# Kernel optimization log

Hardware: AMD Instinct MI355X
Metric: run time of the kernel (lower is better)

The kernel has to match this reference:

```python
import jax, jax.numpy as jnp
import numpy as np

D_MODEL = 768
D_STATE = 16
D_CONV = 4
EXPAND = 2
N_LAYERS = 8
VOCAB = 512
MAXSEQ = 2048
BATCH = 8
SEQ = 2048
D_INNER = EXPAND * D_MODEL
N_EMO, N_STY, N_KEY, N_MODE = 8, 8, 12, 2


def setup_inputs() -> dict:
    key = jax.random.key(0)
    ks = jax.random.split(key, 32)
    def nrm(k, shape, s=0.02):
        return (jax.random.normal(k, shape) * s).astype(jnp.float32)
    inp = {}
    inp['tokens'] = jax.random.randint(ks[0], (BATCH, SEQ), 0, VOCAB)
    inp['emotion'] = jax.random.randint(ks[1], (BATCH,), 0, N_EMO)
    inp['style'] = jax.random.randint(ks[2], (BATCH,), 0, N_STY)
    inp['key_sig'] = jax.random.randint(ks[3], (BATCH,), 0, N_KEY)
    inp['mode'] = jax.random.randint(ks[4], (BATCH,), 0, N_MODE)
    inp['bpm'] = (jax.random.uniform(ks[5], (BATCH,)) * 140.0 + 60.0).astype(jnp.float32)
    inp['tok_emb'] = nrm(ks[6], (VOCAB, D_MODEL))
    inp['emo_emb'] = nrm(ks[7], (N_EMO, D_MODEL))
    inp['sty_emb'] = nrm(ks[8], (N_STY, D_MODEL))
    inp['key_emb'] = nrm(ks[9], (N_KEY, D_MODEL))
    inp['mode_emb'] = nrm(ks[10], (N_MODE, D_MODEL))
    inp['bpm_w'] = nrm(ks[11], (D_MODEL, 1))
    inp['bpm_b'] = jnp.zeros((D_MODEL,), jnp.float32)
    inp['cond_w'] = nrm(ks[12], (D_MODEL, 5 * D_MODEL))
    inp['cond_b'] = jnp.zeros((D_MODEL,), jnp.float32)
    inp['pos_emb'] = nrm(ks[13], (MAXSEQ, D_MODEL))
    inp['ln_g'] = jnp.ones((N_LAYERS, D_MODEL), jnp.float32)
    inp['ln_b'] = jnp.zeros((N_LAYERS, D_MODEL), jnp.float32)
    inp['in_w'] = nrm(ks[14], (N_LAYERS, 2 * D_INNER, D_MODEL))
    inp['conv_w'] = nrm(ks[15], (N_LAYERS, D_INNER, 1, D_CONV), 0.1)
    inp['xproj_w'] = nrm(ks[16], (N_LAYERS, 2 * D_STATE, D_INNER))
    inp['dt_w'] = nrm(ks[17], (N_LAYERS, D_INNER, D_STATE))
    inp['dt_b'] = jnp.zeros((N_LAYERS, D_INNER), jnp.float32)
    inp['bproj_w'] = nrm(ks[18], (N_LAYERS, D_INNER, D_STATE))
    inp['d_param'] = jnp.ones((N_LAYERS, D_INNER), jnp.float32)
    inp['out_w'] = nrm(ks[19], (N_LAYERS, D_MODEL, D_INNER))
    inp['final_g'] = jnp.ones((D_MODEL,), jnp.float32)
    inp['final_b'] = jnp.zeros((D_MODEL,), jnp.float32)
    inp['head_w'] = nrm(ks[20], (VOCAB, D_MODEL))
    inp['head_b'] = jnp.zeros((VOCAB,), jnp.float32)
    return inp


def _layernorm(x, g, b):
    mu = x.mean(-1, keepdims=True)
    v = ((x - mu) ** 2).mean(-1, keepdims=True)
    return (x - mu) * jax.lax.rsqrt(v + 1e-5) * g + b


def _silu(x):
    return x * jax.nn.sigmoid(x)


def _mamba_block(x, in_w, conv_w, xproj_w, dt_w, dt_b, bproj_w, d_param, out_w):
    B, L, _ = x.shape
    xz = x @ in_w.T                       # [B,L,2*di]
    xc, z = jnp.split(xz, 2, axis=-1)
    # causal depthwise conv1d: torch pads d_conv-1 both sides then slices [:L]
    xt = jnp.transpose(xc, (0, 2, 1))     # [B,di,L]
    xt = jax.lax.conv_general_dilated(xt, conv_w, (1,), [(D_CONV - 1, 0)],
                                      feature_group_count=D_INNER)
    xc = _silu(jnp.transpose(xt, (0, 2, 1)))   # [B,L,di]
    dt_raw, b_raw = jnp.split(xc @ xproj_w.T, 2, axis=-1)  # each [B,L,ds]
    delta = jnp.clip(jax.nn.softplus(dt_raw @ dt_w.T + dt_b), 1e-4, 1.0)  # [B,L,di]
    bp = b_raw @ bproj_w.T                 # [B,L,di]

    def step(h, inputs):
        d, u, bb = inputs
        h = h * (1.0 - d) + u * bb
        return h, h

    xs = (jnp.transpose(delta, (1, 0, 2)),
          jnp.transpose(xc, (1, 0, 2)),
          jnp.transpose(bp, (1, 0, 2)))    # time-major [L,B,di]
    h0 = jnp.zeros((B, D_INNER), x.dtype)
    _, ys = jax.lax.scan(step, h0, xs)
    y = jnp.transpose(ys, (1, 0, 2)) + d_param * xc
    y = y * _silu(z)
    return y @ out_w.T


def reference(tokens, emotion, style, key_sig, mode, bpm, tok_emb, emo_emb, sty_emb,
              key_emb, mode_emb, bpm_w, bpm_b, cond_w, cond_b, pos_emb, ln_g, ln_b,
              in_w, conv_w, xproj_w, dt_w, dt_b, bproj_w, d_param, out_w,
              final_g, final_b, head_w, head_b):
    B, L = tokens.shape
    cond = jnp.concatenate([
        emo_emb[emotion], sty_emb[style], key_emb[key_sig], mode_emb[mode],
        bpm[:, None] @ bpm_w.T + bpm_b], axis=-1)       # [B,5d]
    cond = cond @ cond_w.T + cond_b                      # [B,d]
    x = tok_emb[tokens] + cond[:, None, :] + pos_emb[:L][None]
    for i in range(N_LAYERS):
        res = x
        h = _layernorm(x, ln_g[i], ln_b[i])
        x = res + _mamba_block(h, in_w[i], conv_w[i], xproj_w[i], dt_w[i],
                               dt_b[i], bproj_w[i], d_param[i], out_w[i])
    x = _layernorm(x, final_g, final_b)
    return x @ head_w.T + head_b
```

## Files before the change

kernel.cpp:

```cpp
#include <hip/hip_runtime.h>
#include <cstdint>

#define BATCH 8
#define SEQ   2048
#define DM    768
#define DI    1536
#define DS    16
#define NL    8
#define NVOCAB 512
#define BT    (BATCH*SEQ)
#define NCHUNK 32
#define TC    (SEQ/NCHUNK)

typedef __attribute__((ext_vector_type(8))) short bf16x8;
typedef __attribute__((ext_vector_type(4))) float f32x4;

__device__ __forceinline__ unsigned short f2bf(float f){
  unsigned int u = __float_as_uint(f);
  u += 0x7fffu + ((u >> 16) & 1u);
  return (unsigned short)(u >> 16);
}
__device__ __forceinline__ float bf2f(unsigned short s){
  return __uint_as_float(((unsigned int)s) << 16);
}
__device__ __forceinline__ float sigm(float x){ return 1.0f/(1.0f + __expf(-x)); }
__device__ __forceinline__ float siluf(float x){ return x * sigm(x); }
__device__ __forceinline__ float fast_softplus(float x){
  return (x > 15.0f) ? x : __logf(1.0f + __expf(x));
}
__device__ __forceinline__ void async16(void* l, const void* g){
  __builtin_amdgcn_global_load_lds(
      (const __attribute__((address_space(1))) unsigned int*)g,
      (__attribute__((address_space(3))) unsigned int*)l, 16, 0, 0);
}
__device__ __forceinline__ float dot4(f32x4 a, f32x4 b){
  return fmaf(a[0],b[0], fmaf(a[1],b[1], fmaf(a[2],b[2], a[3]*b[3])));
}

__global__ void cvt_bf16_kernel(const float4* __restrict__ in, ushort4* __restrict__ out, int n4){
  int i = blockIdx.x*256 + threadIdx.x;
  int stride = gridDim.x*256;
  for(; i<n4; i+=stride){
    float4 v = in[i];
    ushort4 o; o.x=f2bf(v.x); o.y=f2bf(v.y); o.z=f2bf(v.z); o.w=f2bf(v.w);
    out[i]=o;
  }
}

__global__ __launch_bounds__(256) void cond_kernel(const int* __restrict__ emotion,
    const int* __restrict__ style, const int* __restrict__ keysig, const int* __restrict__ modei,
    const float* __restrict__ bpm, const float* __restrict__ emo_emb, const float* __restrict__ sty_emb,
    const float* __restrict__ key_emb, const float* __restrict__ mode_emb,
    const float* __restrict__ bpm_w, const float* __restrict__ bpm_b,
    const float* __restrict__ cond_w, const float* __restrict__ cond_b,
    float* __restrict__ cond_out){
  int b = blockIdx.y;
  int tid = threadIdx.x;
  __shared__ float vec[5*DM];
  int e = emotion[b], st = style[b], ks = keysig[b], md = modei[b];
  float bp = bpm[b];
  for(int j=tid; j<960; j+=256){
    int seg = j/192, o4 = j - seg*192;
    float4 v;
    if(seg==0)      v = reinterpret_cast<const float4*>(emo_emb + (long)e*DM)[o4];
    else if(seg==1) v = reinterpret_cast<const float4*>(sty_emb + (long)st*DM)[o4];
    else if(seg==2) v = reinterpret_cast<const float4*>(key_emb + (long)ks*DM)[o4];
    else if(seg==3) v = reinterpret_cast<const float4*>(mode_emb + (long)md*DM)[o4];
    else {
      float4 w = reinterpret_cast<const float4*>(bpm_w)[o4];
      float4 bb = reinterpret_cast<const float4*>(bpm_b)[o4];
      v = make_float4(fmaf(bp,w.x,bb.x), fmaf(bp,w.y,bb.y), fmaf(bp,w.z,bb.z), fmaf(bp,w.w,bb.w));
    }
    reinterpret_cast<float4*>(vec)[j] = v;
  }
  __syncthreads();
  int wid = tid>>6, lane = tid&63;
  int dm = blockIdx.x*4 + wid;
  const float4* w4 = reinterpret_cast<const float4*>(cond_w + (long)dm*(5*DM));
  const float4* v4 = reinterpret_cast<const float4*>(vec);
  float acc = 0.f;
  #pragma unroll 5
  for(int j=lane; j<960; j+=64){
    float4 w = w4[j], v = v4[j];
    acc = fmaf(w.x,v.x, fmaf(w.y,v.y, fmaf(w.z,v.z, fmaf(w.w,v.w, acc))));
  }
  #pragma unroll
  for(int off=32; off>0; off>>=1) acc += __shfl_xor(acc, off);
  if(lane==0) cond_out[b*DM + dm] = acc + cond_b[dm];
}

__global__ void embed_kernel(const int* __restrict__ tokens, const float* __restrict__ tok_emb,
    const float* __restrict__ cond, const float* __restrict__ pos_emb, float* __restrict__ x){
  int bt = blockIdx.x;
  int b = bt >> 11, t = bt & 2047;
  int tok = tokens[bt];
  const float4* te = reinterpret_cast<const float4*>(tok_emb + (long)tok*DM);
  const float4* ce = reinterpret_cast<const float4*>(cond + (long)b*DM);
  const float4* pe = reinterpret_cast<const float4*>(pos_emb + (long)t*DM);
  float4* xo = reinterpret_cast<float4*>(x + (long)bt*DM);
  int i = threadIdx.x;
  float4 a = te[i], c = ce[i], p = pe[i];
  xo[i] = make_float4(a.x+c.x+p.x, a.y+c.y+p.y, a.z+c.z+p.z, a.w+c.w+p.w);
}

__global__ __launch_bounds__(256) void ln_bf16_kernel(const float* __restrict__ x,
                     const float* __restrict__ g, const float* __restrict__ bta,
                     unsigned short* __restrict__ out){
  int row  = blockIdx.x*4 + (threadIdx.x >> 6);
  int lane = threadIdx.x & 63;
  const float* xr = x + (long)row*DM;
  float4 v[3];
  float sum=0.f, sq=0.f;
  #pragma unroll
  for(int i=0;i<3;i++){
    v[i] = *reinterpret_cast<const float4*>(xr + i*256 + lane*4);
    sum += v[i].x + v[i].y + v[i].z + v[i].w;
    sq  += v[i].x*v[i].x + v[i].y*v[i].y + v[i].z*v[i].z + v[i].w*v[i].w;
  }
  #pragma unroll
  for(int off=32; off>0; off>>=1){
    sum += __shfl_xor(sum, off);
    sq  += __shfl_xor(sq , off);
  }
  float mu  = sum * (1.0f/DM);
  float var = sq  * (1.0f/DM) - mu*mu;
  float rs  = rsqrtf(var + 1e-5f);
  unsigned short* orow = out + (long)row*DM;
  #pragma unroll
  for(int i=0;i<3;i++){
    int d = i*256 + lane*4;
    float4 gg = *reinterpret_cast<const float4*>(g + d);
    float4 bb = *reinterpret_cast<const float4*>(bta + d);
    ushort4 o;
    o.x = f2bf((v[i].x - mu)*rs*gg.x + bb.x);
    o.y = f2bf((v[i].y - mu)*rs*gg.y + bb.y);
    o.z = f2bf((v[i].z - mu)*rs*gg.z + bb.z);
    o.w = f2bf((v[i].w - mu)*rs*gg.w + bb.w);
    *reinterpret_cast<ushort4*>(orow + d) = o;
  }
}

template<int MODE>
__global__ __launch_bounds__(256) void gemm_lds(const unsigned short* __restrict__ A,
                                               const unsigned short* __restrict__ B,
                                               void* __restrict__ Cv,
                                               const float* __restrict__ bias,
                                               int K, int ldc){
  __shared__ short As[128*64];
  __shared__ short Bs[128*64];
  const short* Ap = (const short*)A;
  const short* Bp = (const short*)B;
  int tid  = threadIdx.x;
  int lane = tid & 63;
  int wid  = tid >> 6;

  int nbx = gridDim.x;
  int id  = blockIdx.y*nbx + blockIdx.x;
  int q   = (nbx*gridDim.y) >> 3;
  int swz = (id & 7)*q + (id >> 3);
  int bx  = swz % nbx, by = swz / nbx;
  int row0 = by*128;
  int col0 = bx*128;

  int srow[4], goff[4];
  #pragma unroll
  for(int j=0;j<4;j++){
    int c = j*256 + tid;
    int row = c>>3, s = c&7;
    srow[j] = row;
    goff[j] = (s ^ (row&7))*8;
  }

  int wr = (wid>>1)*64;
  int wc = (wid&1)*64;
  int fr = lane & 15;
  int kq = lane >> 4;
  int fx = fr & 7;

  f32x4 acc[4][4];
  #pragma unroll
  for(int m=0;m<4;m++)
    #pragma unroll
    for(int n=0;n<4;n++)
      acc[m][n] = (f32x4){0.f,0.f,0.f,0.f};

  for(int kt=0; kt<K; kt+=64){
    #pragma unroll
    for(int j=0;j<4;j++){
      int c = j*256 + tid;
      async16((char*)As + c*16, Ap + (long)(row0+srow[j])*K + kt + goff[j]);
      async16((char*)Bs + c*16, Bp + (long)(col0+srow[j])*K + kt + goff[j]);
    }
    __syncthreads();
    #pragma unroll
    for(int ks=0; ks<2; ks++){
      int sA = ((ks*4 + kq) ^ fx) * 8;
      bf16x8 av[4], bv[4];
      #pragma unroll
      for(int m=0;m<4;m++)
        av[m] = *reinterpret_cast<const bf16x8*>(As + (wr + m*16 + fr)*64 + sA);
      #pragma unroll
      for(int n=0;n<4;n++)
        bv[n] = *reinterpret_cast<const bf16x8*>(Bs + (wc + n*16 + fr)*64 + sA);
      #pragma unroll
      for(int m=0;m<4;m++)
        #pragma unroll
        for(int n=0;n<4;n++)
          acc[m][n] = __builtin_amdgcn_mfma_f32_16x16x32_bf16(av[m], bv[n], acc[m][n], 0, 0, 0);
    }
    __syncthreads();
  }

  int rr = (lane >> 4) << 2;
  int cc = lane & 15;
  #pragma unroll
  for(int m=0;m<4;m++){
    #pragma unroll
    for(int n=0;n<4;n++){
      int col = col0 + wc + n*16 + cc;
      #pragma unroll
      for(int i=0;i<4;i++){
        long idx = (long)(row0 + wr + m*16 + rr + i)*ldc + col;
        float v = acc[m][n][i];
        if(MODE==3)      ((unsigned short*)Cv)[idx] = f2bf(v);
        else if(MODE==1) ((float*)Cv)[idx] += v;
        else if(MODE==2) ((float*)Cv)[idx] = v + bias[col];
        else             ((float*)Cv)[idx] = v;
      }
    }
  }
}

__global__ __launch_bounds__(256) void xproj_kernel(const unsigned short* __restrict__ xz,
      const float* __restrict__ cw, const unsigned short* __restrict__ wbf,
      float* __restrict__ dtb){
  __shared__ unsigned short xcs[16][DI+8];
  __shared__ float pdt[4][16][32];
  int blk = blockIdx.x;
  int b  = blk >> 7;
  int t0 = (blk & 127) << 4;
  int tid = threadIdx.x;
  long base = ((long)b*SEQ + t0)*(2*DI);
  if(tid < 192){
    int d0 = tid*8;
    float cc0[8], cc1[8], cc2[8], cc3[8];
    #pragma unroll
    for(int j=0;j<8;j++){
      cc0[j]=cw[(d0+j)*4+0]; cc1[j]=cw[(d0+j)*4+1];
      cc2[j]=cw[(d0+j)*4+2]; cc3[j]=cw[(d0+j)*4+3];
    }
    float wm3[8], wm2[8], wm1[8];
    #pragma unroll
    for(int j=0;j<8;j++){ wm3[j]=0.f; wm2[j]=0.f; wm1[j]=0.f; }
    if(t0>0){
      bf16x8 v3 = *reinterpret_cast<const bf16x8*>(xz + base - 3*(2*DI) + d0);
      bf16x8 v2 = *reinterpret_cast<const bf16x8*>(xz + base - 2*(2*DI) + d0);
      bf16x8 v1 = *reinterpret_cast<const bf16x8*>(xz + base - 1*(2*DI) + d0);
      #pragma unroll
      for(int j=0;j<8;j++){
        wm3[j]=bf2f((unsigned short)v3[j]);
        wm2[j]=bf2f((unsigned short)v2[j]);
        wm1[j]=bf2f((unsigned short)v1[j]);
      }
    }
    for(int tt=0; tt<16; tt++){
      bf16x8 vt = *reinterpret_cast<const bf16x8*>(xz + base + (long)tt*(2*DI) + d0);
      bf16x8 o;
      #pragma unroll
      for(int j=0;j<8;j++){
        float wt = bf2f((unsigned short)vt[j]);
        float u  = cc0[j]*wm3[j] + cc1[j]*wm2[j] + cc2[j]*wm1[j] + cc3[j]*wt;
        o[j] = (short)f2bf(siluf(u));
        wm3[j]=wm2[j]; wm2[j]=wm1[j]; wm1[j]=wt;
      }
      *reinterpret_cast<bf16x8*>(&xcs[tt][d0]) = o;
    }
  }
  __syncthreads();
  int wid = tid >> 6, lane = tid & 63;
  int fr = lane & 15, kq = lane >> 4;
  f32x4 a0 = (f32x4){0.f,0.f,0.f,0.f};
  f32x4 a1 = (f32x4){0.f,0.f,0.f,0.f};
  const unsigned short* w0 = wbf + (long)fr*DI;
  const unsigned short* w1 = wbf + (long)(16+fr)*DI;
  int kbase = wid*384 + kq*8;
  #pragma unroll
  for(int ks=0; ks<12; ks++){
    int k = kbase + ks*32;
    bf16x8 av = *reinterpret_cast<const bf16x8*>(&xcs[fr][k]);
    bf16x8 b0 = *reinterpret_cast<const bf16x8*>(w0 + k);
    bf16x8 b1 = *reinterpret_cast<const bf16x8*>(w1 + k);
    a0 = __builtin_amdgcn_mfma_f32_16x16x32_bf16(av, b0, a0, 0, 0, 0);
    a1 = __builtin_amdgcn_mfma_f32_16x16x32_bf16(av, b1, a1, 0, 0, 0);
  }
  int rr = kq << 2;
  #pragma unroll
  for(int i=0;i<4;i++){
    pdt[wid][rr+i][fr]      = a0[i];
    pdt[wid][rr+i][16+fr]   = a1[i];
  }
  __syncthreads();
  for(int e = tid; e < 512; e += 256){
    int r = e >> 5, s = e & 31;
    float v = pdt[0][r][s] + pdt[1][r][s] + pdt[2][r][s] + pdt[3][r][s];
    dtb[((long)b*SEQ + t0 + r)*32 + s] = v;
  }
}

__global__ __launch_bounds__(256) void scanAY_kernel(const unsigned short* __restrict__ xz,
      const float* __restrict__ dtb, const float* __restrict__ cw,
      const float* __restrict__ dtw_g, const float* __restrict__ dtbias_g,
      const float* __restrict__ bpw_g, const float* __restrict__ dp_g,
      float2* __restrict__ chunk, unsigned short* __restrict__ y,
      unsigned short* __restrict__ asz_s){
  __shared__ float dsb[TC*32];
  int c = blockIdx.x, db = blockIdx.y, b = blockIdx.z;
  int d = db*256 + threadIdx.x;
  int t0 = c*TC;
  {
    const float4* src = reinterpret_cast<const float4*>(dtb + ((long)b*SEQ + t0)*32);
    float4* dst = reinterpret_cast<float4*>(dsb);
    dst[threadIdx.x]       = src[threadIdx.x];
    dst[threadIdx.x + 256] = src[threadIdx.x + 256];
  }
  float c0=cw[d*4],c1=cw[d*4+1],c2=cw[d*4+2],c3=cw[d*4+3];
  f32x4 wq0 = *reinterpret_cast<const f32x4*>(dtw_g + d*16 + 0);
  f32x4 wq1 = *reinterpret_cast<const f32x4*>(dtw_g + d*16 + 4);
  f32x4 wq2 = *reinterpret_cast<const f32x4*>(dtw_g + d*16 + 8);
  f32x4 wq3 = *reinterpret_cast<const f32x4*>(dtw_g + d*16 + 12);
  f32x4 wp0 = *reinterpret_cast<const f32x4*>(bpw_g + d*16 + 0);
  f32x4 wp1 = *reinterpret_cast<const f32x4*>(bpw_g + d*16 + 4);
  f32x4 wp2 = *reinterpret_cast<const f32x4*>(bpw_g + d*16 + 8);
  f32x4 wp3 = *reinterpret_cast<const f32x4*>(bpw_g + d*16 + 12);
  float bias = dtbias_g[d];
  float dp = dp_g[d];
  asm volatile("" : "+v"(wq0),"+v"(wq1),"+v"(wq2),"+v"(wq3),
                    "+v"(wp0),"+v"(wp1),"+v"(wp2),"+v"(wp3),
                    "+v"(c0),"+v"(c1),"+v"(c2),"+v"(c3),"+v"(bias),"+v"(dp));
  long base = ((long)b*SEQ + t0)*(2*DI) + d;
  float wm3 = (t0>0) ? bf2f(xz[base - 3*(2*DI)]) : 0.f;
  float wm2 = (t0>0) ? bf2f(xz[base - 2*(2*DI)]) : 0.f;
  float wm1 = (t0>0) ? bf2f(xz[base - 1*(2*DI)]) : 0.f;
  const unsigned short* xp = xz + base;
  const unsigned short* zp = xz + base + DI;
  long sidx = ((long)b*SEQ + t0)*DI + d;
  unsigned short* yp = y + sidx;
  unsigned short* ap = asz_s + sidx;
  __syncthreads();
  float h = 0.f, P = 1.f;
  for(int g=0; g<TC/8; g++){
    unsigned short xv[8], zv[8];
    #pragma unroll
    for(int j=0;j<8;j++){ xv[j] = xp[(long)j*2*DI]; zv[j] = zp[(long)j*2*DI]; }
    xp += 8L*2*DI; zp += 8L*2*DI;
    const float* rp = dsb + g*8*32;
    #pragma unroll
    for(int j=0;j<8;j++){
      float wt = bf2f(xv[j]);
      float u = siluf(fmaf(c3,wt, fmaf(c2,wm1, fmaf(c1,wm2, c0*wm3))));
      wm3=wm2; wm2=wm1; wm1=wt;
      const f32x4* row = reinterpret_cast<const f32x4*>(rp + j*32);
      float da = bias + dot4(row[0],wq0) + dot4(row[1],wq1) + dot4(row[2],wq2) + dot4(row[3],wq3);
      float ba =        dot4(row[4],wp0) + dot4(row[5],wp1) + dot4(row[6],wp2) + dot4(row[7],wp3);
      float delta = fminf(fmaxf(fast_softplus(da), 1e-4f), 1.0f);
      float a = 1.0f - delta;
      h = fmaf(h, a, u*ba);
      P *= a;
      float sz = siluf(bf2f(zv[j]));
      yp[(long)j*DI] = f2bf(fmaf(dp, u, h) * sz);
      ap[(long)j*DI] = f2bf(P * sz);
    }
    yp += 8L*DI; ap += 8L*DI;
  }
  chunk[((long)b*DI + d)*NCHUNK + c] = make_float2(P, h);
}

__global__ __launch_bounds__(256) void h0_kernel(const float2* __restrict__ chunk,
                                                 float* __restrict__ h0tab){
  int idx = blockIdx.x*256 + threadIdx.x;
  int b = idx / DI, d = idx - b*DI;
  const float2* cb = chunk + ((long)b*DI + d)*NCHUNK;
  float h0 = 0.f;
  for(int c=0; c<NCHUNK; c++){
    h0tab[((long)b*NCHUNK + c)*DI + d] = h0;
    float2 ps = cb[c];
    h0 = fmaf(ps.x, h0, ps.y);
  }
}

__global__ __launch_bounds__(256) void fixup_kernel(const unsigned short* __restrict__ asz_s,
      const float* __restrict__ h0tab, unsigned short* __restrict__ y){
  int i = (blockIdx.x*256 + threadIdx.x)*8;
  int bt = i / DI;
  int d  = i - bt*DI;
  int b  = bt >> 11;
  int c  = (bt & 2047) >> 6;
  const float* hp = h0tab + ((long)b*NCHUNK + c)*DI + d;
  f32x4 h0a = *reinterpret_cast<const f32x4*>(hp);
  f32x4 h0b = *reinterpret_cast<const f32x4*>(hp + 4);
  bf16x8 yv = *reinterpret_cast<const bf16x8*>(y + i);
  bf16x8 av = *reinterpret_cast<const bf16x8*>(asz_s + i);
  bf16x8 o;
  #pragma unroll
  for(int j=0;j<8;j++){
    float h0 = (j<4) ? h0a[j] : h0b[j-4];
    o[j] = (short)f2bf(fmaf(h0, bf2f((unsigned short)av[j]), bf2f((unsigned short)yv[j])));
  }
  *reinterpret_cast<bf16x8*>(y + i) = o;
}

__global__ __launch_bounds__(256) void scanA_kernel(const unsigned short* __restrict__ xz,
      const float* __restrict__ dtb, const float* __restrict__ cw,
      const float* __restrict__ dtw_g, const float* __restrict__ dtbias_g,
      const float* __restrict__ bpw_g, float2* __restrict__ chunk){
  __shared__ float dsb[TC*32];
  int c = blockIdx.x, db = blockIdx.y, b = blockIdx.z;
  int d = db*256 + threadIdx.x;
  int t0 = c*TC;
  {
    const float4* src = reinterpret_cast<const float4*>(dtb + ((long)b*SEQ + t0)*32);
    float4* dst = reinterpret_cast<float4*>(dsb);
    dst[threadIdx.x]       = src[threadIdx.x];
    dst[threadIdx.x + 256] = src[threadIdx.x + 256];
  }
  float c0=cw[d*4],c1=cw[d*4+1],c2=cw[d*4+2],c3=cw[d*4+3];
  f32x4 wq0 = *reinterpret_cast<const f32x4*>(dtw_g + d*16 + 0);
  f32x4 wq1 = *reinterpret_cast<const f32x4*>(dtw_g + d*16 + 4);
  f32x4 wq2 = *reinterpret_cast<const f32x4*>(dtw_g + d*16 + 8);
  f32x4 wq3 = *reinterpret_cast<const f32x4*>(dtw_g + d*16 + 12);
  f32x4 wp0 = *reinterpret_cast<const f32x4*>(bpw_g + d*16 + 0);
  f32x4 wp1 = *reinterpret_cast<const f32x4*>(bpw_g + d*16 + 4);
  f32x4 wp2 = *reinterpret_cast<const f32x4*>(bpw_g + d*16 + 8);
  f32x4 wp3 = *reinterpret_cast<const f32x4*>(bpw_g + d*16 + 12);
  float bias = dtbias_g[d];
  asm volatile("" : "+v"(wq0),"+v"(wq1),"+v"(wq2),"+v"(wq3),
                    "+v"(wp0),"+v"(wp1),"+v"(wp2),"+v"(wp3),
                    "+v"(c0),"+v"(c1),"+v"(c2),"+v"(c3),"+v"(bias));
  long base = ((long)b*SEQ + t0)*(2*DI) + d;
  float wm3 = (t0>0) ? bf2f(xz[base - 3*(2*DI)]) : 0.f;
  float wm2 = (t0>0) ? bf2f(xz[base - 2*(2*DI)]) : 0.f;
  float wm1 = (t0>0) ? bf2f(xz[base - 1*(2*DI)]) : 0.f;
  const unsigned short* xp = xz + base;
  __syncthreads();
  float h = 0.f, P = 1.f;
  for(int t=0;t<TC;t++){
    float wt = bf2f(*xp); xp += 2*DI;
    float u = siluf(fmaf(c3,wt, fmaf(c2,wm1, fmaf(c1,wm2, c0*wm3))));
    wm3=wm2; wm2=wm1; wm1=wt;
    const f32x4* row = reinterpret_cast<const f32x4*>(dsb + t*32);
    float da = bias + dot4(row[0],wq0) + dot4(row[1],wq1) + dot4(row[2],wq2) + dot4(row[3],wq3);
    float ba =        dot4(row[4],wp0) + dot4(row[5],wp1) + dot4(row[6],wp2) + dot4(row[7],wp3);
    float delta = fminf(fmaxf(fast_softplus(da), 1e-4f), 1.0f);
    float a = 1.0f - delta;
    h = fmaf(h, a, u*ba);
    P *= a;
  }
  chunk[((long)b*DI + d)*NCHUNK + c] = make_float2(P, h);
}

__global__ __launch_bounds__(256) void scanC_heavy_kernel(const unsigned short* __restrict__ xz,
      const float* __restrict__ dtb, const float* __restrict__ cw,
      const float* __restrict__ dtw_g, const float* __restrict__ dtbias_g,
      const float* __restrict__ bpw_g, const float* __restrict__ dp_g,
      const float2* __restrict__ chunk, unsigned short* __restrict__ y){
  __shared__ float dsb[TC*32];
  int c = blockIdx.x, db = blockIdx.y, b = blockIdx.z;
  int d = db*256 + threadIdx.x;
  int t0 = c*TC;
  {
    const float4* src = reinterpret_cast<const float4*>(dtb + ((long)b*SEQ + t0)*32);
    float4* dst = reinterpret_cast<float4*>(dsb);
    dst[threadIdx.x]       = src[threadIdx.x];
    dst[threadIdx.x + 256] = src[threadIdx.x + 256];
  }
  float c0=cw[d*4],c1=cw[d*4+1],c2=cw[d*4+2],c3=cw[d*4+3];
  f32x4 wq0 = *reinterpret_cast<const f32x4*>(dtw_g + d*16 + 0);
  f32x4 wq1 = *reinterpret_cast<const f32x4*>(dtw_g + d*16 + 4);
  f32x4 wq2 = *reinterpret_cast<const f32x4*>(dtw_g + d*16 + 8);
  f32x4 wq3 = *reinterpret_cast<const f32x4*>(dtw_g + d*16 + 12);
  f32x4 wp0 = *reinterpret_cast<const f32x4*>(bpw_g + d*16 + 0);
  f32x4 wp1 = *reinterpret_cast<const f32x4*>(bpw_g + d*16 + 4);
  f32x4 wp2 = *reinterpret_cast<const f32x4*>(bpw_g + d*16 + 8);
  f32x4 wp3 = *reinterpret_cast<const f32x4*>(bpw_g + d*16 + 12);
  float bias = dtbias_g[d];
  float dp = dp_g[d];
  asm volatile("" : "+v"(wq0),"+v"(wq1),"+v"(wq2),"+v"(wq3),
                    "+v"(wp0),"+v"(wp1),"+v"(wp2),"+v"(wp3),
                    "+v"(c0),"+v"(c1),"+v"(c2),"+v"(c3),"+v"(bias),"+v"(dp));
  long base = ((long)b*SEQ + t0)*(2*DI) + d;
  float wm3 = (t0>0) ? bf2f(xz[base - 3*(2*DI)]) : 0.f;
  float wm2 = (t0>0) ? bf2f(xz[base - 2*(2*DI)]) : 0.f;
  float wm1 = (t0>0) ? bf2f(xz[base - 1*(2*DI)]) : 0.f;
  const unsigned short* xp = xz + base;
  const unsigned short* zp = xz + base + DI;
  unsigned short* yp = y + ((long)b*SEQ + t0)*DI + d;
  float h = 0.f;
  const float2* cb = chunk + ((long)b*DI + d)*NCHUNK;
  for(int cc2=0; cc2<c; cc2++){ float2 ps = cb[cc2]; h = ps.x*h + ps.y; }
  __syncthreads();
  for(int t=0;t<TC;t++){
    float wt = bf2f(*xp); xp += 2*DI;
    float u = siluf(fmaf(c3,wt, fmaf(c2,wm1, fmaf(c1,wm2, c0*wm3))));
    wm3=wm2; wm2=wm1; wm1=wt;
    const f32x4* row = reinterpret_cast<const f32x4*>(dsb + t*32);
    float da = bias + dot4(row[0],wq0) + dot4(row[1],wq1) + dot4(row[2],wq2) + dot4(row[3],wq3);
    float ba =        dot4(row[4],wp0) + dot4(row[5],wp1) + dot4(row[6],wp2) + dot4(row[7],wp3);
    float delta = fminf(fmaxf(fast_softplus(da), 1e-4f), 1.0f);
    h = fmaf(h, 1.0f - delta, u*ba);
    float zv = bf2f(*zp); zp += 2*DI;
    float yv = (h + dp*u) * siluf(zv);
    *yp = f2bf(yv); yp += DI;
  }
}

extern "C" void kernel_launch(void* const* d_in, const int* in_sizes, int n_in,
                              void* d_out, int out_size, void* d_ws, size_t ws_size,
                              hipStream_t stream){
  const int*   tokens  = (const int*)  d_in[0];
  const int*   emotion = (const int*)  d_in[1];
  const int*   style   = (const int*)  d_in[2];
  const int*   keysig  = (const int*)  d_in[3];
  const int*   modei   = (const int*)  d_in[4];
  const float* bpm     = (const float*)d_in[5];
  const float* tok_emb = (const float*)d_in[6];
  const float* emo_emb = (const float*)d_in[7];
  const float* sty_emb = (const float*)d_in[8];
  const float* key_emb = (const float*)d_in[9];
  const float* mode_emb= (const float*)d_in[10];
  const float* bpm_w   = (const float*)d_in[11];
  const float* bpm_b   = (const float*)d_in[12];
  const float* cond_w  = (const float*)d_in[13];
  const float* cond_b  = (const float*)d_in[14];
  const float* pos_emb = (const float*)d_in[15];
  const float* ln_g    = (const float*)d_in[16];
  const float* ln_b    = (const float*)d_in[17];
  const float* in_w    = (const float*)d_in[18];
  const float* conv_w  = (const float*)d_in[19];
  const float* xproj_w = (const float*)d_in[20];
  const float* dt_w    = (const float*)d_in[21];
  const float* dt_b    = (const float*)d_in[22];
  const float* bproj_w = (const float*)d_in[23];
  const float* d_param = (const float*)d_in[24];
  const float* out_w   = (const float*)d_in[25];
  const float* final_g = (const float*)d_in[26];
  const float* final_b = (const float*)d_in[27];
  const float* head_w  = (const float*)d_in[28];
  const float* head_b  = (const float*)d_in[29];

  char* ws = (char*)d_ws;
  float*          x       = (float*)(ws + 0L);
  unsigned short* hy      = (unsigned short*)(ws + 50331648L);
  unsigned short* xz      = (unsigned short*)(ws + 100663296L);
  float*          dtbuf   = (float*)(ws + 201326592L);
  float2*         chunk   = (float2*)(ws + 203423744L);
  float*          condv   = (float*)(ws + 206569472L);
  unsigned short* inwb    = (unsigned short*)(ws + 206594048L);
  unsigned short* outwb   = (unsigned short*)(ws + 211312640L);
  unsigned short* headwb  = (unsigned short*)(ws + 213671936L);
  unsigned short* wbf_all = (unsigned short*)(ws + 214458368L);
  float*          h0tab   = (float*)(ws + 215244800L);
  unsigned short* asz_s   = (unsigned short*)(ws + 216817664L);

  const bool use_y0 = (ws_size >= 267149312UL);

  unsigned short* h_bf = hy;
  unsigned short* y_bf = hy;
  unsigned short* xfin = hy;

  cvt_bf16_kernel<<<128,256,0,stream>>>((const float4*)head_w,(ushort4*)headwb, NVOCAB*DM/4);
  cvt_bf16_kernel<<<384,256,0,stream>>>((const float4*)xproj_w,(ushort4*)wbf_all, NL*32*DI/4);
  cond_kernel<<<dim3(DM/4,8),256,0,stream>>>(emotion, style, keysig, modei, bpm, emo_emb, sty_emb,
        key_emb, mode_emb, bpm_w, bpm_b, cond_w, cond_b, condv);
  embed_kernel<<<BT,192,0,stream>>>(tokens, tok_emb, condv, pos_emb, x);

  for(int l=0; l<NL; l++){
    cvt_bf16_kernel<<<1024,256,0,stream>>>((const float4*)(in_w  + (long)l*2*DI*DM), (ushort4*)inwb,  2*DI*DM/4);
    cvt_bf16_kernel<<<512, 256,0,stream>>>((const float4*)(out_w + (long)l*DM*DI),   (ushort4*)outwb, DM*DI/4);
    ln_bf16_kernel<<<BT/4,256,0,stream>>>(x, ln_g + l*DM, ln_b + l*DM, h_bf);
    gemm_lds<3><<<dim3(2*DI/128, BT/128),256,0,stream>>>(h_bf, inwb, xz, nullptr, DM, 2*DI);
    xproj_kernel<<<BT/16,256,0,stream>>>(xz, conv_w + l*DI*4, wbf_all + (long)l*32*DI, dtbuf);
    if(use_y0){
      scanAY_kernel<<<dim3(NCHUNK,6,BATCH),256,0,stream>>>(xz, dtbuf, conv_w + l*DI*4,
            dt_w + l*DI*DS, dt_b + l*DI, bproj_w + l*DI*DS, d_param + l*DI, chunk, y_bf, asz_s);
      h0_kernel<<<48,256,0,stream>>>(chunk, h0tab);
      fixup_kernel<<<BT*DI/(256*8),256,0,stream>>>(asz_s, h0tab, y_bf);
    } else {
      scanA_kernel<<<dim3(NCHUNK,6,BATCH),256,0,stream>>>(xz, dtbuf, conv_w + l*DI*4,
            dt_w + l*DI*DS, dt_b + l*DI, bproj_w + l*DI*DS, chunk);
      scanC_heavy_kernel<<<dim3(NCHUNK,6,BATCH),256,0,stream>>>(xz, dtbuf, conv_w + l*DI*4,
            dt_w + l*DI*DS, dt_b + l*DI, bproj_w + l*DI*DS, d_param + l*DI, chunk, y_bf);
    }
    gemm_lds<1><<<dim3(DM/128, BT/128),256,0,stream>>>(y_bf, outwb, x, nullptr, DI, DM);
  }
  ln_bf16_kernel<<<BT/4,256,0,stream>>>(x, final_g, final_b, xfin);
  gemm_lds<2><<<dim3(NVOCAB/128, BT/128),256,0,stream>>>(xfin, headwb, d_out, head_b, DM, NVOCAB);
}
```

Measured before the change: 2.686 ms.

## Compute scan delta/B projections with MFMA and fuse SiLU(z) gate into fixup

Adds a scan kernel that computes the per-timestep dt and B projections for a 64-step chunk with bf16 MFMA into LDS. This replaces the per-thread 32-wide fp32 dot products inside the sequential loop. The SiLU(z) gating moves into the fixup pass. Weights are pre-packed into a combined bf16 buffer, which lowers precision of da/ba to bf16. The path only runs when the workspace is large enough, and the old scanA/scanC fallback is removed.

```diff
diff --git a/kernel.cpp b/kernel.cpp
--- a/kernel.cpp
+++ b/kernel.cpp
@@ -45,6 +45,14 @@
     ushort4 o; o.x=f2bf(v.x); o.y=f2bf(v.y); o.z=f2bf(v.z); o.w=f2bf(v.w);
     out[i]=o;
   }
+}
+
+__global__ void wcomb_kernel(const float* __restrict__ dt_w, const float* __restrict__ bproj_w,
+                             unsigned short* __restrict__ out){
+  int idx = blockIdx.x*256 + threadIdx.x;
+  int k = idx & 31, ld = idx >> 5;
+  float v = (k < 16) ? dt_w[(long)ld*16 + k] : bproj_w[(long)ld*16 + (k-16)];
+  out[idx] = f2bf(v);
 }
 
 __global__ __launch_bounds__(256) void cond_kernel(const int* __restrict__ emotion,
@@ -305,6 +313,96 @@
     float v = pdt[0][r][s] + pdt[1][r][s] + pdt[2][r][s] + pdt[3][r][s];
     dtb[((long)b*SEQ + t0 + r)*32 + s] = v;
   }
+}
+
+__global__ __launch_bounds__(256) void scanAY_mfma_kernel(const unsigned short* __restrict__ xz,
+      const float* __restrict__ dtb, const float* __restrict__ cw,
+      const unsigned short* __restrict__ wcomb,
+      const float* __restrict__ dtbias_g, const float* __restrict__ dp_g,
+      float2* __restrict__ chunk, unsigned short* __restrict__ y0s,
+      unsigned short* __restrict__ as_s){
+  __shared__ unsigned short abuf[64][32];
+  __shared__ unsigned short dab[64*256*2];
+  int c = blockIdx.x, db = blockIdx.y, b = blockIdx.z;
+  int tid = threadIdx.x;
+  int t0 = c*TC;
+  {
+    const float4* src = reinterpret_cast<const float4*>(dtb + ((long)b*SEQ + t0)*32);
+    float4 v0 = src[tid*2], v1 = src[tid*2+1];
+    bf16x8 o;
+    o[0]=(short)f2bf(v0.x); o[1]=(short)f2bf(v0.y); o[2]=(short)f2bf(v0.z); o[3]=(short)f2bf(v0.w);
+    o[4]=(short)f2bf(v1.x); o[5]=(short)f2bf(v1.y); o[6]=(short)f2bf(v1.z); o[7]=(short)f2bf(v1.w);
+    *reinterpret_cast<bf16x8*>(&abuf[tid>>2][(tid&3)*8]) = o;
+  }
+  __syncthreads();
+  {
+    int w = tid >> 6, lane = tid & 63;
+    int fr = lane & 15, kq = lane >> 4;
+    bf16x8 zero = {0,0,0,0,0,0,0,0};
+    bf16x8 bq[4], bp[4];
+    #pragma unroll
+    for(int nt=0; nt<4; nt++){
+      int dcol = db*256 + w*64 + nt*16 + fr;
+      bf16x8 wv = *reinterpret_cast<const bf16x8*>(wcomb + (long)dcol*32 + kq*8);
+      bq[nt] = (kq<2) ? wv : zero;
+      bp[nt] = (kq<2) ? zero : wv;
+    }
+    #pragma unroll
+    for(int mt=0; mt<4; mt++){
+      bf16x8 av = *reinterpret_cast<const bf16x8*>(&abuf[mt*16 + fr][kq*8]);
+      #pragma unroll
+      for(int nt=0; nt<4; nt++){
+        f32x4 aq = __builtin_amdgcn_mfma_f32_16x16x32_bf16(av, bq[nt], (f32x4){0.f,0.f,0.f,0.f}, 0,0,0);
+        f32x4 ap = __builtin_amdgcn_mfma_f32_16x16x32_bf16(av, bp[nt], (f32x4){0.f,0.f,0.f,0.f}, 0,0,0);
+        int dl = w*64 + nt*16 + fr;
+        #pragma unroll
+        for(int i=0;i<4;i++){
+          int t = mt*16 + kq*4 + i;
+          unsigned int pack = (unsigned int)f2bf(aq[i]) | (((unsigned int)f2bf(ap[i]))<<16);
+          *reinterpret_cast<unsigned int*>(&dab[(t*256 + dl)*2]) = pack;
+        }
+      }
+    }
+  }
+  int d = db*256 + tid;
+  float c0=cw[d*4],c1=cw[d*4+1],c2=cw[d*4+2],c3=cw[d*4+3];
+  float bias = dtbias_g[d];
+  float dp = dp_g[d];
+  asm volatile("" : "+v"(c0),"+v"(c1),"+v"(c2),"+v"(c3),"+v"(bias),"+v"(dp));
+  long base = ((long)b*SEQ + t0)*(2*DI) + d;
+  float wm3 = (t0>0) ? bf2f(xz[base - 3*(2*DI)]) : 0.f;
+  float wm2 = (t0>0) ? bf2f(xz[base - 2*(2*DI)]) : 0.f;
+  float wm1 = (t0>0) ? bf2f(xz[base - 1*(2*DI)]) : 0.f;
+  const unsigned short* xp = xz + base;
+  long sidx = ((long)b*SEQ + t0)*DI + d;
+  unsigned short* yp = y0s + sidx;
+  unsigned short* ap2 = as_s + sidx;
+  __syncthreads();
+  float h = 0.f, P = 1.f;
+  const unsigned int* dab32 = reinterpret_cast<const unsigned int*>(dab);
+  for(int g=0; g<TC/8; g++){
+    unsigned short xv[8];
+    #pragma unroll
+    for(int j=0;j<8;j++){ xv[j] = xp[(long)j*2*DI]; }
+    xp += 8L*2*DI;
+    #pragma unroll
+    for(int j=0;j<8;j++){
+      float wt = bf2f(xv[j]);
+      float u = siluf(fmaf(c3,wt, fmaf(c2,wm1, fmaf(c1,wm2, c0*wm3))));
+      wm3=wm2; wm2=wm1; wm1=wt;
+      unsigned int pk = dab32[(g*8+j)*256 + tid];
+      float da = bias + bf2f((unsigned short)(pk & 0xffffu));
+      float ba = bf2f((unsigned short)(pk >> 16));
+      float delta = fminf(fmaxf(fast_softplus(da), 1e-4f), 1.0f);
+      float a = 1.0f - delta;
+      h = fmaf(h, a, u*ba);
+      P *= a;
+      yp[(long)j*DI]  = f2bf(fmaf(dp, u, h));
+      ap2[(long)j*DI] = f2bf(P);
+    }
+    yp += 8L*DI; ap2 += 8L*DI;
+  }
+  chunk[((long)b*DI + d)*NCHUNK + c] = make_float2(P, h);
 }
 
 __global__ __launch_bounds__(256) void scanAY_kernel(const unsigned short* __restrict__ xz,
@@ -388,6 +486,30 @@
   }
 }
 
+__global__ __launch_bounds__(256) void fixup_z_kernel(const unsigned short* __restrict__ as_s,
+      const float* __restrict__ h0tab, const unsigned short* __restrict__ xz,
+      unsigned short* __restrict__ y){
+  int i = (blockIdx.x*256 + threadIdx.x)*8;
+  int bt = i / DI;
+  int d  = i - bt*DI;
+  int b  = bt >> 11;
+  int c  = (bt & 2047) >> 6;
+  const float* hp = h0tab + ((long)b*NCHUNK + c)*DI + d;
+  f32x4 h0a = *reinterpret_cast<const f32x4*>(hp);
+  f32x4 h0b = *reinterpret_cast<const f32x4*>(hp + 4);
+  bf16x8 yv = *reinterpret_cast<const bf16x8*>(y + i);
+  bf16x8 av = *reinterpret_cast<const bf16x8*>(as_s + i);
+  bf16x8 zv = *reinterpret_cast<const bf16x8*>(xz + (long)bt*(2*DI) + DI + d);
+  bf16x8 o;
+  #pragma unroll
+  for(int j=0;j<8;j++){
+    float h0 = (j<4) ? h0a[j] : h0b[j-4];
+    float v = fmaf(h0, bf2f((unsigned short)av[j]), bf2f((unsigned short)yv[j]));
+    o[j] = (short)f2bf(v * siluf(bf2f((unsigned short)zv[j])));
+  }
+  *reinterpret_cast<bf16x8*>(y + i) = o;
+}
+
 __global__ __launch_bounds__(256) void fixup_kernel(const unsigned short* __restrict__ asz_s,
       const float* __restrict__ h0tab, unsigned short* __restrict__ y){
   int i = (blockIdx.x*256 + threadIdx.x)*8;
@@ -407,110 +529,6 @@
     o[j] = (short)f2bf(fmaf(h0, bf2f((unsigned short)av[j]), bf2f((unsigned short)yv[j])));
   }
   *reinterpret_cast<bf16x8*>(y + i) = o;
-}
-
-__global__ __launch_bounds__(256) void scanA_kernel(const unsigned short* __restrict__ xz,
-      const float* __restrict__ dtb, const float* __restrict__ cw,
-      const float* __restrict__ dtw_g, const float* __restrict__ dtbias_g,
-      const float* __restrict__ bpw_g, float2* __restrict__ chunk){
-  __shared__ float dsb[TC*32];
-  int c = blockIdx.x, db = blockIdx.y, b = blockIdx.z;
-  int d = db*256 + threadIdx.x;
-  int t0 = c*TC;
-  {
-    const float4* src = reinterpret_cast<const float4*>(dtb + ((long)b*SEQ + t0)*32);
-    float4* dst = reinterpret_cast<float4*>(dsb);
-    dst[threadIdx.x]       = src[threadIdx.x];
-    dst[threadIdx.x + 256] = src[threadIdx.x + 256];
-  }
-  float c0=cw[d*4],c1=cw[d*4+1],c2=cw[d*4+2],c3=cw[d*4+3];
-  f32x4 wq0 = *reinterpret_cast<const f32x4*>(dtw_g + d*16 + 0);
-  f32x4 wq1 = *reinterpret_cast<const f32x4*>(dtw_g + d*16 + 4);
-  f32x4 wq2 = *reinterpret_cast<const f32x4*>(dtw_g + d*16 + 8);
-  f32x4 wq3 = *reinterpret_cast<const f32x4*>(dtw_g + d*16 + 12);
-  f32x4 wp0 = *reinterpret_cast<const f32x4*>(bpw_g + d*16 + 0);
-  f32x4 wp1 = *reinterpret_cast<const f32x4*>(bpw_g + d*16 + 4);
-  f32x4 wp2 = *reinterpret_cast<const f32x4*>(bpw_g + d*16 + 8);
-  f32x4 wp3 = *reinterpret_cast<const f32x4*>(bpw_g + d*16 + 12);
-  float bias = dtbias_g[d];
-  asm volatile("" : "+v"(wq0),"+v"(wq1),"+v"(wq2),"+v"(wq3),
-                    "+v"(wp0),"+v"(wp1),"+v"(wp2),"+v"(wp3),
-                    "+v"(c0),"+v"(c1),"+v"(c2),"+v"(c3),"+v"(bias));
-  long base = ((long)b*SEQ + t0)*(2*DI) + d;
-  float wm3 = (t0>0) ? bf2f(xz[base - 3*(2*DI)]) : 0.f;
-  float wm2 = (t0>0) ? bf2f(xz[base - 2*(2*DI)]) : 0.f;
-  float wm1 = (t0>0) ? bf2f(xz[base - 1*(2*DI)]) : 0.f;
-  const unsigned short* xp = xz + base;
-  __syncthreads();
-  float h = 0.f, P = 1.f;
-  for(int t=0;t<TC;t++){
-    float wt = bf2f(*xp); xp += 2*DI;
-    float u = siluf(fmaf(c3,wt, fmaf(c2,wm1, fmaf(c1,wm2, c0*wm3))));
-    wm3=wm2; wm2=wm1; wm1=wt;
-    const f32x4* row = reinterpret_cast<const f32x4*>(dsb + t*32);
-    float da = bias + dot4(row[0],wq0) + dot4(row[1],wq1) + dot4(row[2],wq2) + dot4(row[3],wq3);
-    float ba =        dot4(row[4],wp0) + dot4(row[5],wp1) + dot4(row[6],wp2) + dot4(row[7],wp3);
-    float delta = fminf(fmaxf(fast_softplus(da), 1e-4f), 1.0f);
-    float a = 1.0f - delta;
-    h = fmaf(h, a, u*ba);
-    P *= a;
-  }
-  chunk[((long)b*DI + d)*NCHUNK + c] = make_float2(P, h);
-}
-
-__global__ __launch_bounds__(256) void scanC_heavy_kernel(const unsigned short* __restrict__ xz,
-      const float* __restrict__ dtb, const float* __restrict__ cw,
-      const float* __restrict__ dtw_g, const float* __restrict__ dtbias_g,
-      const float* __restrict__ bpw_g, const float* __restrict__ dp_g,
-      const float2* __restrict__ chunk, unsigned short* __restrict__ y){
-  __shared__ float dsb[TC*32];
-  int c = blockIdx.x, db = blockIdx.y, b = blockIdx.z;
-  int d = db*256 + threadIdx.x;
-  int t0 = c*TC;
-  {
-    const float4* src = reinterpret_cast<const float4*>(dtb + ((long)b*SEQ + t0)*32);
-    float4* dst = reinterpret_cast<float4*>(dsb);
-    dst[threadIdx.x]       = src[threadIdx.x];
-    dst[threadIdx.x + 256] = src[threadIdx.x + 256];
-  }
-  float c0=cw[d*4],c1=cw[d*4+1],c2=cw[d*4+2],c3=cw[d*4+3];
-  f32x4 wq0 = *reinterpret_cast<const f32x4*>(dtw_g + d*16 + 0);
-  f32x4 wq1 = *reinterpret_cast<const f32x4*>(dtw_g + d*16 + 4);
-  f32x4 wq2 = *reinterpret_cast<const f32x4*>(dtw_g + d*16 + 8);
-  f32x4 wq3 = *reinterpret_cast<const f32x4*>(dtw_g + d*16 + 12);
-  f32x4 wp0 = *reinterpret_cast<const f32x4*>(bpw_g + d*16 + 0);
-  f32x4 wp1 = *reinterpret_cast<const f32x4*>(bpw_g + d*16 + 4);
-  f32x4 wp2 = *reinterpret_cast<const f32x4*>(bpw_g + d*16 + 8);
-  f32x4 wp3 = *reinterpret_cast<const f32x4*>(bpw_g + d*16 + 12);
-  float bias = dtbias_g[d];
-  float dp = dp_g[d];
-  asm volatile("" : "+v"(wq0),"+v"(wq1),"+v"(wq2),"+v"(wq3),
-                    "+v"(wp0),"+v"(wp1),"+v"(wp2),"+v"(wp3),
-                    "+v"(c0),"+v"(c1),"+v"(c2),"+v"(c3),"+v"(bias),"+v"(dp));
-  long base = ((long)b*SEQ + t0)*(2*DI) + d;
-  float wm3 = (t0>0) ? bf2f(xz[base - 3*(2*DI)]) : 0.f;
-  float wm2 = (t0>0) ? bf2f(xz[base - 2*(2*DI)]) : 0.f;
-  float wm1 = (t0>0) ? bf2f(xz[base - 1*(2*DI)]) : 0.f;
-  const unsigned short* xp = xz + base;
-  const unsigned short* zp = xz + base + DI;
-  unsigned short* yp = y + ((long)b*SEQ + t0)*DI + d;
-  float h = 0.f;
-  const float2* cb = chunk + ((long)b*DI + d)*NCHUNK;
-  for(int cc2=0; cc2<c; cc2++){ float2 ps = cb[cc2]; h = ps.x*h + ps.y; }
-  __syncthreads();
-  for(int t=0;t<TC;t++){
-    float wt = bf2f(*xp); xp += 2*DI;
-    float u = siluf(fmaf(c3,wt, fmaf(c2,wm1, fmaf(c1,wm2, c0*wm3))));
-    wm3=wm2; wm2=wm1; wm1=wt;
-    const f32x4* row = reinterpret_cast<const f32x4*>(dsb + t*32);
-    float da = bias + dot4(row[0],wq0) + dot4(row[1],wq1) + dot4(row[2],wq2) + dot4(row[3],wq3);
-    float ba =        dot4(row[4],wp0) + dot4(row[5],wp1) + dot4(row[6],wp2) + dot4(row[7],wp3);
-    float delta = fminf(fmaxf(fast_softplus(da), 1e-4f), 1.0f);
-    h = fmaf(h, 1.0f - delta, u*ba);
-    float zv = bf2f(*zp); zp += 2*DI;
-    float yv = (h + dp*u) * siluf(zv);
-    *yp = f2bf(yv); yp += DI;
-  }
 }
 
 extern "C" void kernel_launch(void* const* d_in, const int* in_sizes, int n_in,
@@ -560,8 +578,10 @@
   unsigned short* wbf_all = (unsigned short*)(ws + 214458368L);
   float*          h0tab   = (float*)(ws + 215244800L);
   unsigned short* asz_s   = (unsigned short*)(ws + 216817664L);
-
-  const bool use_y0 = (ws_size >= 267149312UL);
+  unsigned short* wcombb  = (unsigned short*)(ws + 267149312L);
+
+  const bool use_y0   = (ws_size >= 267149312UL);
+  const bool use_mfma = (ws_size >= 267935744UL);
 
   unsigned short* h_bf = hy;
   unsigned short* y_bf = hy;
@@ -569,6 +589,8 @@
 
   cvt_bf16_kernel<<<128,256,0,stream>>>((const float4*)head_w,(ushort4*)headwb, NVOCAB*DM/4);
   cvt_bf16_kernel<<<384,256,0,stream>>>((const float4*)xproj_w,(ushort4*)wbf_all, NL*32*DI/4);
+  if(use_mfma)
+    wcomb_kernel<<<NL*DI*32/256,256,0,stream>>>(dt_w, bproj_w, wcombb);
   cond_kernel<<<dim3(DM/4,8),256,0,stream>>>(emotion, style, keysig, modei, bpm, emo_emb, sty_emb,
         key_emb, mode_emb, bpm_w, bpm_b, cond_w, cond_b, condv);
   embed_kernel<<<BT,192,0,stream>>>(tokens, tok_emb, condv, pos_emb, x);
@@ -579,16 +601,16 @@
     ln_bf16_kernel<<<BT/4,256,0,stream>>>(x, ln_g + l*DM, ln_b + l*DM, h_bf);
     gemm_lds<3><<<dim3(2*DI/128, BT/128),256,0,stream>>>(h_bf, inwb, xz, nullptr, DM, 2*DI);
     xproj_kernel<<<BT/16,256,0,stream>>>(xz, conv_w + l*DI*4, wbf_all + (long)l*32*DI, dtbuf);
-    if(use_y0){
+    if(use_mfma){
+      scanAY_mfma_kernel<<<dim3(NCHUNK,6,BATCH),256,0,stream>>>(xz, dtbuf, conv_w + l*DI*4,
+            wcombb + (long)l*DI*32, dt_b + l*DI, d_param + l*DI, chunk, y_bf, asz_s);
+      h0_kernel<<<48,256,0,stream>>>(chunk, h0tab);
+      fixup_z_kernel<<<BT*DI/(256*8),256,0,stream>>>(asz_s, h0tab, xz, y_bf);
+    } else {
       scanAY_kernel<<<dim3(NCHUNK,6,BATCH),256,0,stream>>>(xz, dtbuf, conv_w + l*DI*4,
             dt_w + l*DI*DS, dt_b + l*DI, bproj_w + l*DI*DS, d_param + l*DI, chunk, y_bf, asz_s);
       h0_kernel<<<48,256,0,stream>>>(chunk, h0tab);
       fixup_kernel<<<BT*DI/(256*8),256,0,stream>>>(asz_s, h0tab, y_bf);
-    } else {
-      scanA_kernel<<<dim3(NCHUNK,6,BATCH),256,0,stream>>>(xz, dtbuf, conv_w + l*DI*4,
-            dt_w + l*DI*DS, dt_b + l*DI, bproj_w + l*DI*DS, chunk);
-      scanC_heavy_kernel<<<dim3(NCHUNK,6,BATCH),256,0,stream>>>(xz, dtbuf, conv_w + l*DI*4,
-            dt_w + l*DI*DS, dt_b + l*DI, bproj_w + l*DI*DS, d_param + l*DI, chunk, y_bf);
     }
     gemm_lds<1><<<dim3(DM/128, BT/128),256,0,stream>>>(y_bf, outwb, x, nullptr, DI, DM);
   }
```

After: 2.381 ms. 1.13x faster.
